# Kernel optimization log

Hardware: AMD Instinct MI355X
Metric: run time of the kernel (lower is better)

The kernel has to match this reference:

```python
import jax, jax.numpy as jnp
import numpy as np

SCALES = [3, 5, 7, 9]


def _conv1d(x, w, b, k):
    # x: (BN, 1, L), w: (1, 1, k), b: (1,) -> (BN, 1, L), 'same' padding (k//2)
    y = jax.lax.conv_general_dilated(
        x, w, window_strides=(1,), padding=[(k // 2, k // 2)],
        dimension_numbers=("NCH", "OIH", "NCH"))
    return y + b[None, :, None]


def setup_inputs() -> dict:
    key = jax.random.key(0)
    ks = jax.random.split(key, 16)
    B, N, L = 64, 321, 720
    inp = {"x": jax.random.normal(ks[0], (B, N, L), dtype=jnp.float32)}
    # Conv1d(1,1,k) params, kaiming-ish scale 1/sqrt(k)
    for i, s in enumerate(SCALES):
        inp[f"cw{i}"] = jax.random.normal(ks[1 + 2 * i], (1, 1, s), dtype=jnp.float32) / np.sqrt(s)
        inp[f"cb{i}"] = jax.random.normal(ks[2 + 2 * i], (1,), dtype=jnp.float32) * 0.01
    # weight_net: Linear(4,32) -> ReLU -> Linear(32,4) -> Softmax
    inp["W1"] = jax.random.normal(ks[10], (4, 32), dtype=jnp.float32) / np.sqrt(4.0)
    inp["b1"] = jnp.zeros((32,), dtype=jnp.float32)
    inp["W2"] = jax.random.normal(ks[11], (32, 4), dtype=jnp.float32) / np.sqrt(32.0)
    inp["b2"] = jnp.zeros((4,), dtype=jnp.float32)
    return inp


def reference(x, cw0, cb0, cw1, cb1, cw2, cb2, cw3, cb3, W1, b1, W2, b2):
    B, N, L = x.shape
    xf = x.reshape(B * N, 1, L)
    cparams = [(cw0, cb0), (cw1, cb1), (cw2, cb2), (cw3, cb3)]
    feats, ents = [], []
    for (w, b), k in zip(cparams, SCALES):
        f = _conv1d(xf, w, b, k)                      # (BN, 1, L)
        prob = jax.nn.softmax(f, axis=-1)
        ent = -(prob * jnp.log(prob + 1e-8)).sum(axis=-1)  # (BN, 1)
        feats.append(f)
        ents.append(ent)
    entropy_vec = jnp.concatenate(ents, axis=-1)      # (BN, 4)
    h = jax.nn.relu(entropy_vec @ W1 + b1)
    weights = jax.nn.softmax(h @ W2 + b2, axis=-1)    # (BN, 4)
    stacked = jnp.stack(feats, axis=1)                # (BN, 4, 1, L)
    trend = (stacked * weights[:, :, None, None]).sum(axis=1)  # (BN, 1, L)
    return trend.reshape(B, N, L)
```

## Files before the change

kernel.cpp:

```cpp
#include <hip/hip_runtime.h>
#include <math.h>

#define NT 256
#define L_LEN 720
#define NROWS (64 * 321)

#define LOG2E 1.4426950408889634f
#define LN2   0.6931471805599453f

__global__ __launch_bounds__(NT, 8) void trend_kernel(
    const float* __restrict__ x,
    const float* __restrict__ cw0, const float* __restrict__ cb0,
    const float* __restrict__ cw1, const float* __restrict__ cb1,
    const float* __restrict__ cw2, const float* __restrict__ cb2,
    const float* __restrict__ cw3, const float* __restrict__ cb3,
    const float* __restrict__ W1, const float* __restrict__ b1,
    const float* __restrict__ W2, const float* __restrict__ b2,
    float* __restrict__ out)
{
    const int lane = threadIdx.x & 63;
    const int wid  = threadIdx.x >> 6;
    const int row  = blockIdx.x * 4 + wid;

    const float* __restrict__ xr = x + (size_t)row * L_LEN;

    const float* cws[4] = {cw0, cw1, cw2, cw3};
    const float* cbs[4] = {cb0, cb1, cb2, cb3};
    float w[4][9], bias[4];
#pragma unroll
    for (int s = 0; s < 4; ++s) {
        const int k = 3 + 2 * s;
        bias[s] = cbs[s][0];
#pragma unroll
        for (int t = 0; t < 9; ++t) w[s][t] = (t < k) ? cws[s][t] : 0.0f;
    }

    const bool active = lane < 60;

    float xw[20];
    float S[4]  = {0.f, 0.f, 0.f, 0.f};
    float Tu[4] = {0.f, 0.f, 0.f, 0.f};

    if (active) {
        const int e0 = 12 * lane - 4;
#pragma unroll
        for (int q = 0; q < 5; ++q) {
            int e = e0 + 4 * q;
            e = (e < 0) ? 0 : ((e > L_LEN - 4) ? (L_LEN - 4) : e);
            float4 v = *(const float4*)(xr + e);
            xw[4 * q + 0] = v.x; xw[4 * q + 1] = v.y;
            xw[4 * q + 2] = v.z; xw[4 * q + 3] = v.w;
        }
        if (lane == 0)  { xw[0] = 0.f; xw[1] = 0.f; xw[2] = 0.f; xw[3] = 0.f; }
        if (lane == 59) { xw[16] = 0.f; xw[17] = 0.f; xw[18] = 0.f; xw[19] = 0.f; }

#pragma unroll
        for (int e = 0; e < 12; ++e) {
#pragma unroll
            for (int s = 0; s < 4; ++s) {
                const int k = 3 + 2 * s;
                const int off = 3 - s;
                float acc = bias[s];
#pragma unroll
                for (int u = 0; u < k; ++u)
                    acc = fmaf(w[s][u], xw[e + off + u], acc);
                float uu = acc * LOG2E;
                float ev = __builtin_amdgcn_exp2f(uu);
                S[s]  += ev;
                Tu[s]  = fmaf(uu, ev, Tu[s]);
            }
        }
    }

#pragma unroll
    for (int s = 0; s < 4; ++s) {
#pragma unroll
        for (int off = 32; off; off >>= 1) {
            S[s]  += __shfl_xor(S[s],  off);
            Tu[s] += __shfl_xor(Tu[s], off);
        }
    }

    float ent[4];
#pragma unroll
    for (int s = 0; s < 4; ++s) {
        float r = __builtin_amdgcn_rcpf(S[s]);
        ent[s] = LN2 * (__builtin_amdgcn_logf(S[s]) - Tu[s] * r);
    }

    const int hidx = lane & 31;
    float h = b1[hidx];
#pragma unroll
    for (int s = 0; s < 4; ++s) h = fmaf(ent[s], W1[s * 32 + hidx], h);
    h = fmaxf(h, 0.0f);

    const float4 w2v = ((const float4*)W2)[hidx];
    float lg[4] = {h * w2v.x, h * w2v.y, h * w2v.z, h * w2v.w};
#pragma unroll
    for (int c = 0; c < 4; ++c) {
#pragma unroll
        for (int off = 16; off; off >>= 1)
            lg[c] += __shfl_xor(lg[c], off);
    }
    lg[0] += b2[0]; lg[1] += b2[1]; lg[2] += b2[2]; lg[3] += b2[3];

    float m = fmaxf(fmaxf(lg[0], lg[1]), fmaxf(lg[2], lg[3]));
    float e0w = __expf(lg[0] - m), e1w = __expf(lg[1] - m);
    float e2w = __expf(lg[2] - m), e3w = __expf(lg[3] - m);
    float inv = 1.0f / (e0w + e1w + e2w + e3w);
    const float wgt[4] = {e0w * inv, e1w * inv, e2w * inv, e3w * inv};

    float Wm[9] = {0.f, 0.f, 0.f, 0.f, 0.f, 0.f, 0.f, 0.f, 0.f};
    float Bm = 0.f;
#pragma unroll
    for (int s = 0; s < 4; ++s) {
        const int k = 3 + 2 * s;
        const int off = 3 - s;
#pragma unroll
        for (int u = 0; u < k; ++u)
            Wm[off + u] = fmaf(wgt[s], w[s][u], Wm[off + u]);
        Bm = fmaf(wgt[s], bias[s], Bm);
    }

    if (active) {
        float* __restrict__ orow = out + (size_t)row * L_LEN + 12 * lane;
#pragma unroll
        for (int q = 0; q < 3; ++q) {
            float4 v;
#pragma unroll
            for (int c = 0; c < 4; ++c) {
                const int e = 4 * q + c;
                float acc = Bm;
#pragma unroll
                for (int j = 0; j < 9; ++j)
                    acc = fmaf(Wm[j], xw[e + j], acc);
                ((float*)&v)[c] = acc;
            }
            *(float4*)(orow + 4 * q) = v;
        }
    }
}

extern "C" void kernel_launch(void* const* d_in, const int* in_sizes, int n_in,
                              void* d_out, int out_size, void* d_ws, size_t ws_size,
                              hipStream_t stream) {
    const float* xp  = (const float*)d_in[0];
    const float* cw0 = (const float*)d_in[1];
    const float* cb0 = (const float*)d_in[2];
    const float* cw1 = (const float*)d_in[3];
    const float* cb1 = (const float*)d_in[4];
    const float* cw2 = (const float*)d_in[5];
    const float* cb2 = (const float*)d_in[6];
    const float* cw3 = (const float*)d_in[7];
    const float* cb3 = (const float*)d_in[8];
    const float* W1  = (const float*)d_in[9];
    const float* b1  = (const float*)d_in[10];
    const float* W2  = (const float*)d_in[11];
    const float* b2  = (const float*)d_in[12];
    float* outp = (float*)d_out;

    trend_kernel<<<NROWS / 4, NT, 0, stream>>>(xp, cw0, cb0, cw1, cb1, cw2, cb2,
                                               cw3, cb3, W1, b1, W2, b2, outp);
}
```

Baseline: 39.40 us.

## Split fused kernel into entropy-weight kernel and separate output convolution kernel

Splits the single fused kernel into two launches. The first computes the per-row entropies, the gating weights and a combined 9-tap filter plus bias, and writes them to workspace. The second kernel applies that combined filter with one thread per 4 output elements, for fully coalesced, evenly spread output writes. In exchange, the input is read twice, a second launch is added, and there is a small workspace round trip.

```diff
diff --git a/kernel.cpp b/kernel.cpp
--- a/kernel.cpp
+++ b/kernel.cpp
@@ -4,11 +4,14 @@
 #define NT 256
 #define L_LEN 720
 #define NROWS (64 * 321)
+#define CHUNKS_PER_ROW 180
+#define NCHUNK (NROWS * CHUNKS_PER_ROW)
+#define WM_STRIDE 12
 
 #define LOG2E 1.4426950408889634f
 #define LN2   0.6931471805599453f
 
-__global__ __launch_bounds__(NT, 8) void trend_kernel(
+__global__ __launch_bounds__(NT, 8) void ent_kernel(
     const float* __restrict__ x,
     const float* __restrict__ cw0, const float* __restrict__ cb0,
     const float* __restrict__ cw1, const float* __restrict__ cb1,
@@ -16,7 +19,7 @@
     const float* __restrict__ cw3, const float* __restrict__ cb3,
     const float* __restrict__ W1, const float* __restrict__ b1,
     const float* __restrict__ W2, const float* __restrict__ b2,
-    float* __restrict__ out)
+    float* __restrict__ wm)
 {
     const int lane = threadIdx.x & 63;
     const int wid  = threadIdx.x >> 6;
@@ -37,12 +40,12 @@
 
     const bool active = lane < 60;
 
-    float xw[20];
     float S[4]  = {0.f, 0.f, 0.f, 0.f};
     float Tu[4] = {0.f, 0.f, 0.f, 0.f};
 
     if (active) {
         const int e0 = 12 * lane - 4;
+        float xw[20];
 #pragma unroll
         for (int q = 0; q < 5; ++q) {
             int e = e0 + 4 * q;
@@ -83,10 +86,9 @@
 
     float ent[4];
 #pragma unroll
-    for (int s = 0; s < 4; ++s) {
-        float r = __builtin_amdgcn_rcpf(S[s]);
-        ent[s] = LN2 * (__builtin_amdgcn_logf(S[s]) - Tu[s] * r);
-    }
+    for (int s = 0; s < 4; ++s)
+        ent[s] = LN2 * (__builtin_amdgcn_logf(S[s])
+                        - Tu[s] * __builtin_amdgcn_rcpf(S[s]));
 
     const int hidx = lane & 31;
     float h = b1[hidx];
@@ -110,7 +112,7 @@
     float inv = 1.0f / (e0w + e1w + e2w + e3w);
     const float wgt[4] = {e0w * inv, e1w * inv, e2w * inv, e3w * inv};
 
-    float Wm[9] = {0.f, 0.f, 0.f, 0.f, 0.f, 0.f, 0.f, 0.f, 0.f};
+    float Wm[9] = {0,0,0,0,0,0,0,0,0};
     float Bm = 0.f;
 #pragma unroll
     for (int s = 0; s < 4; ++s) {
@@ -122,23 +124,61 @@
         Bm = fmaf(wgt[s], bias[s], Bm);
     }
 
-    if (active) {
-        float* __restrict__ orow = out + (size_t)row * L_LEN + 12 * lane;
-#pragma unroll
-        for (int q = 0; q < 3; ++q) {
-            float4 v;
-#pragma unroll
-            for (int c = 0; c < 4; ++c) {
-                const int e = 4 * q + c;
-                float acc = Bm;
-#pragma unroll
-                for (int j = 0; j < 9; ++j)
-                    acc = fmaf(Wm[j], xw[e + j], acc);
-                ((float*)&v)[c] = acc;
-            }
-            *(float4*)(orow + 4 * q) = v;
-        }
-    }
+    if (lane == 0) {
+        float* __restrict__ dst = wm + (size_t)row * WM_STRIDE;
+        float4 a = {Wm[0], Wm[1], Wm[2], Wm[3]};
+        float4 b = {Wm[4], Wm[5], Wm[6], Wm[7]};
+        float2 c = {Wm[8], Bm};
+        *(float4*)(dst)     = a;
+        *(float4*)(dst + 4) = b;
+        *(float2*)(dst + 8) = c;
+    }
+}
+
+__global__ __launch_bounds__(NT) void out_kernel(
+    const float* __restrict__ x,
+    const float* __restrict__ wm,
+    float* __restrict__ out)
+{
+    const int c = blockIdx.x * NT + threadIdx.x;
+    const int r  = c / CHUNKS_PER_ROW;
+    const int j4 = (c - r * CHUNKS_PER_ROW) * 4;
+
+    const float* __restrict__ xr = x + (size_t)r * L_LEN;
+    const float* __restrict__ wr = wm + (size_t)r * WM_STRIDE;
+
+    const float4 wa = *(const float4*)(wr);
+    const float4 wb = *(const float4*)(wr + 4);
+    const float2 wc = *(const float2*)(wr + 8);
+    const float W[9] = {wa.x, wa.y, wa.z, wa.w, wb.x, wb.y, wb.z, wb.w, wc.x};
+    const float Bm = wc.y;
+
+    float xv[12];
+    if (j4 >= 4 && j4 <= L_LEN - 8) {
+        float4 A = *(const float4*)(xr + j4 - 4);
+        float4 B = *(const float4*)(xr + j4);
+        float4 C = *(const float4*)(xr + j4 + 4);
+        xv[0] = A.x; xv[1] = A.y; xv[2]  = A.z; xv[3]  = A.w;
+        xv[4] = B.x; xv[5] = B.y; xv[6]  = B.z; xv[7]  = B.w;
+        xv[8] = C.x; xv[9] = C.y; xv[10] = C.z; xv[11] = C.w;
+    } else {
+#pragma unroll
+        for (int t = 0; t < 12; ++t) {
+            const int e = j4 - 4 + t;
+            xv[t] = (e >= 0 && e < L_LEN) ? xr[e] : 0.0f;
+        }
+    }
+
+    float4 o;
+#pragma unroll
+    for (int c0 = 0; c0 < 4; ++c0) {
+        float acc = Bm;
+#pragma unroll
+        for (int d = 0; d < 9; ++d)
+            acc = fmaf(W[d], xv[c0 + d], acc);
+        ((float*)&o)[c0] = acc;
+    }
+    *(float4*)(out + (size_t)r * L_LEN + j4) = o;
 }
 
 extern "C" void kernel_launch(void* const* d_in, const int* in_sizes, int n_in,
@@ -158,7 +198,9 @@
     const float* W2  = (const float*)d_in[11];
     const float* b2  = (const float*)d_in[12];
     float* outp = (float*)d_out;
-
-    trend_kernel<<<NROWS / 4, NT, 0, stream>>>(xp, cw0, cb0, cw1, cb1, cw2, cb2,
-                                               cw3, cb3, W1, b1, W2, b2, outp);
+    float* wm   = (float*)d_ws;
+
+    ent_kernel<<<NROWS / 4, NT, 0, stream>>>(xp, cw0, cb0, cw1, cb1, cw2, cb2,
+                                             cw3, cb3, W1, b1, W2, b2, wm);
+    out_kernel<<<NCHUNK / NT, NT, 0, stream>>>(xp, wm, outp);
 }
```

After: 75.13 us. 1.91x slower.
